# Kernel tuning notes

Measured on AMD Instinct MI355X. Metric: run time of the kernel, lower is better.

Reference implementation:

```python
import jax, jax.numpy as jnp
import numpy as np

KS = 5
STRIDE = 1


def extract_patches(x, ks, s):
    # TF tf.image.extract_patches ordering: (row, col, channel) flattened
    B, H, W, C = x.shape
    oh = (H - ks) // s + 1
    ow = (W - ks) // s + 1
    cols = [x[:, i:i + (oh - 1) * s + 1:s, j:j + (ow - 1) * s + 1:s, :]
            for i in range(ks) for j in range(ks)]
    p = jnp.stack(cols, axis=3)  # [B, oh, ow, ks*ks, C]
    return p.reshape(B, oh * ow, ks * ks * C)


def setup_inputs() -> dict:
    key = jax.random.key(0)
    k1, k2, k3 = jax.random.split(key, 3)
    B, H, W, C, K = 32, 14, 14, 32, 64
    mu_in = jax.random.normal(k1, (B, H, W, C), dtype=jnp.float32)
    Sigma_in = jax.random.uniform(k2, (B, H * W, H * W, C), dtype=jnp.float32)
    w_mu = 0.05 * jax.random.normal(k3, (KS, KS, C, K), dtype=jnp.float32)
    w_sigma = jnp.full((K,), -2.2, dtype=jnp.float32)
    return {"mu_in": mu_in, "Sigma_in": Sigma_in, "w_mu": w_mu, "w_sigma": w_sigma}


def reference(mu_in, Sigma_in, w_mu, w_sigma):
    B, H, W, C = mu_in.shape
    ks = w_mu.shape[0]
    K = w_mu.shape[-1]
    s = STRIDE

    # mean path: standard conv2d, NHWC / HWIO
    mu_out = jax.lax.conv_general_dilated(
        mu_in, w_mu, (s, s), 'VALID',
        dimension_numbers=('NHWC', 'HWIO', 'NHWC'))

    # diag of Sigma_in over the two N dims: [B,N,N,C] -> [B,C,N] -> [B,H,W,C]
    diag_sigma = jnp.diagonal(Sigma_in, axis1=1, axis2=2)           # [B,C,N]
    diag_sigma = jnp.transpose(diag_sigma, (0, 2, 1)).reshape(B, H, W, C)

    dsg = extract_patches(diag_sigma, ks, s)                        # [B,P,M]
    P = dsg.shape[1]

    mu_cov_sq = (w_mu * w_mu).reshape(-1, K)                        # [M,K]
    v1 = dsg @ mu_cov_sq                                            # [B,P,K]

    sp = jnp.log1p(jnp.exp(w_sigma))                                # softplus, [K]
    tr = jnp.sum(dsg, axis=2, keepdims=True)                        # [B,P,1]
    diag_vals = v1 + sp[None, None, :] * tr                         # [B,P,K] (trace1 + mu_wT_sigmags_mu_w diags)

    mu_p = extract_patches(mu_in, ks, s)                            # [B,P,M]
    G = jnp.einsum('bpm,bqm->bpq', mu_p, mu_p)                      # [B,P,P]

    Sigma_out = sp[None, None, None, :] * G[..., None]              # [B,P,P,K]
    ip = jnp.arange(P)
    Sigma_out = Sigma_out.at[:, ip, ip, :].add(diag_vals)

    Sigma_out = jnp.where(jnp.isnan(Sigma_out), 0.0, Sigma_out)
    Sigma_out = jnp.where(jnp.isinf(Sigma_out), 0.0, Sigma_out)

    # TF set_diag acts on the LAST two dims ([P,K] inner matrices) -- reproduce exactly
    m = min(P, K)
    ii = jnp.arange(m)
    Sigma_out = Sigma_out.at[:, :, ii, ii].set(jnp.abs(Sigma_out[:, :, ii, ii]))
    return mu_out, Sigma_out
```

## Files before the change

kernel.cpp:

```cpp
#include <hip/hip_runtime.h>
#include <cmath>

typedef __attribute__((ext_vector_type(8))) short short8;
typedef __attribute__((ext_vector_type(4))) float f32x4;

#define NB 32
#define PP 100
#define KK 64
#define MU_OUT_SZ (NB*PP*KK)
#define LDAP 56

__device__ inline unsigned short f2bf(float f) {
  unsigned u = __builtin_bit_cast(unsigned, f);
  u += 0x7fffu + ((u >> 16) & 1u);
  return (unsigned short)(u >> 16);
}

__global__ __launch_bounds__(256) void prepW(
    const float* __restrict__ w_mu, const float* __restrict__ w_sigma,
    unsigned short* __restrict__ wf) {
  const int wid = blockIdx.x * 256 + threadIdx.x;
  const int kind = wid >= 6400 ? 1 : 0;
  const int fid = kind ? wid - 6400 : wid;
  const int ij = fid >> 8;
  const int rest = fid & 255;
  const int n = rest >> 6, l = rest & 63;
  const int col = n * 16 + (l & 15);
  const int m0 = ij * 32 + (l >> 4) * 8;
  const float sp = log1pf(expf(w_sigma[col]));
  unsigned short v[8];
#pragma unroll
  for (int i = 0; i < 8; ++i) {
    float wv = w_mu[(m0 + i) * 64 + col];
    float x = kind ? (wv * wv + sp) : wv;
    v[i] = f2bf(x);
  }
  uint4 pk;
  pk.x = v[0] | ((unsigned)v[1] << 16);
  pk.y = v[2] | ((unsigned)v[3] << 16);
  pk.z = v[4] | ((unsigned)v[5] << 16);
  pk.w = v[6] | ((unsigned)v[7] << 16);
  *(uint4*)(wf + (size_t)((ij * 8 + kind * 4 + n) * 64 + l) * 8) = pk;
}

__global__ __launch_bounds__(256) void fused(
    const float* __restrict__ mu_in, const float* __restrict__ Sigma_in,
    const float* __restrict__ w_sigma, const unsigned short* __restrict__ wf,
    float* __restrict__ out) {
  __shared__ unsigned short mu_sh[196 * LDAP];
  __shared__ unsigned short sd_sh[196 * LDAP];
  __shared__ float g_sh[16][100];
  __shared__ float dv_sh[16][64];
  const int r = blockIdx.x;
  const int zh = blockIdx.y;
  const int b = blockIdx.z;
  const int t = threadIdx.x, l = t & 63, w = t >> 6;
  const int laneP = l & 15, g16 = (l >> 4) * 8;
  const bool hasDv = (zh == 0) ? (r <= 3) : (r >= 4);

  const float4* mu4 = (const float4*)(mu_in + (size_t)b * 6272);
  for (int f = t; f < 1568; f += 256) {
    const float4 v = mu4[f];
    const int row = f >> 3, c = (f & 7) * 4;
    ushort4 pv;
    pv.x = f2bf(v.x); pv.y = f2bf(v.y); pv.z = f2bf(v.z); pv.w = f2bf(v.w);
    *(ushort4*)(mu_sh + row * LDAP + c) = pv;
  }
  if (hasDv) {
    for (int f = t; f < 1568; f += 256) {
      const int n = f >> 3, c = (f & 7) * 4;
      const float4 v = *(const float4*)(Sigma_in +
          ((size_t)(b * 196 + n) * 196 + n) * 32 + c);
      ushort4 pv;
      pv.x = f2bf(v.x); pv.y = f2bf(v.y); pv.z = f2bf(v.z); pv.w = f2bf(v.w);
      *(ushort4*)(sd_sh + n * LDAP + c) = pv;
    }
  }
  __syncthreads();

  const int gTile = (zh == 0) ? w : (w < 3 ? 4 + w : -1);
  const bool doMu = (zh == 1);
  const int nT = w;

  int pA = r * 16 + laneP; if (pA > 99) pA = 99;
  const int baseA = ((pA / 10) * 14 + (pA % 10)) * LDAP + g16;
  int gcol = 0, baseB = 0;
  if (gTile >= 0) {
    gcol = gTile * 16 + laneP;
    const int pc = gcol > 99 ? 99 : gcol;
    baseB = ((pc / 10) * 14 + (pc % 10)) * LDAP + g16;
  }
  f32x4 accG = {}, accM = {}, accD = {};
#pragma unroll
  for (int ij = 0; ij < 25; ++ij) {
    const int off = ((ij / 5) * 14 + (ij % 5)) * LDAP;
    const short8 fA = *(const short8*)(mu_sh + baseA + off);
    if (gTile >= 0) {
      const short8 fB = *(const short8*)(mu_sh + baseB + off);
      accG = __builtin_amdgcn_mfma_f32_16x16x32_bf16(fA, fB, accG, 0, 0, 0);
    }
    if (doMu) {
      const short8 bw = *(const short8*)(wf + (size_t)((ij * 8 + nT) * 64 + l) * 8);
      accM = __builtin_amdgcn_mfma_f32_16x16x32_bf16(fA, bw, accM, 0, 0, 0);
    }
    if (hasDv) {
      const short8 fS = *(const short8*)(sd_sh + baseA + off);
      const short8 b2 = *(const short8*)(wf + (size_t)((ij * 8 + 4 + nT) * 64 + l) * 8);
      accD = __builtin_amdgcn_mfma_f32_16x16x32_bf16(fS, b2, accD, 0, 0, 0);
    }
  }
  const int prow0 = (l >> 4) * 4;
  if (gTile >= 0 && gcol < 100) {
#pragma unroll
    for (int j = 0; j < 4; ++j) g_sh[prow0 + j][gcol] = accG[j];
  }
  if (doMu) {
    float* mo = out + (size_t)b * 6400;
    const int k = nT * 16 + laneP;
#pragma unroll
    for (int j = 0; j < 4; ++j) {
      const int p = r * 16 + prow0 + j;
      if (p < 100) mo[p * 64 + k] = accM[j];
    }
  }
  if (hasDv) {
    const int k = nT * 16 + laneP;
#pragma unroll
    for (int j = 0; j < 4; ++j) dv_sh[prow0 + j][k] = accD[j];
  }
  __syncthreads();

  const int nrows = (r == 6) ? 4 : 16;
  const int koff = (t & 15) * 4;
  const float4 wsv = *(const float4*)(w_sigma + koff);
  float4 sp4;
  sp4.x = log1pf(expf(wsv.x));
  sp4.y = log1pf(expf(wsv.y));
  sp4.z = log1pf(expf(wsv.z));
  sp4.w = log1pf(expf(wsv.w));
  const int p0 = r * 16;
  float* sig = out + MU_OUT_SZ + ((size_t)(b * 100 + p0) * 100) * 64;

  if (zh == 0) {
    const int total = nrows << 10;
    for (int l4 = t; l4 < total; l4 += 256) {
      const int prow = l4 >> 10, rem = l4 & 1023;
      const int q = rem >> 4;
      const float g = g_sh[prow][q];
      float4 v;
      v.x = sp4.x * g; v.y = sp4.y * g; v.z = sp4.z * g; v.w = sp4.w * g;
      if (q == p0 + prow) {
        const float4 dvv = *(const float4*)&dv_sh[prow][koff];
        v.x += dvv.x; v.y += dvv.y; v.z += dvv.z; v.w += dvv.w;
      }
      if (q == koff)     v.x = fabsf(v.x);
      if (q == koff + 1) v.y = fabsf(v.y);
      if (q == koff + 2) v.z = fabsf(v.z);
      if (q == koff + 3) v.w = fabsf(v.w);
      *(float4*)(sig + ((size_t)prow * 100 + q) * 64 + koff) = v;
    }
  } else {
    const int total = nrows * 576;
    for (int l4 = t; l4 < total; l4 += 256) {
      const int prow = l4 / 576, rem = l4 - prow * 576;
      const int q = 64 + (rem >> 4);
      const float g = g_sh[prow][q];
      float4 v;
      v.x = sp4.x * g; v.y = sp4.y * g; v.z = sp4.z * g; v.w = sp4.w * g;
      if (q == p0 + prow) {
        const float4 dvv = *(const float4*)&dv_sh[prow][koff];
        v.x += dvv.x; v.y += dvv.y; v.z += dvv.z; v.w += dvv.w;
      }
      *(float4*)(sig + ((size_t)prow * 100 + q) * 64 + koff) = v;
    }
  }
}

extern "C" void kernel_launch(void* const* d_in, const int* in_sizes, int n_in,
                              void* d_out, int out_size, void* d_ws, size_t ws_size,
                              hipStream_t stream) {
  const float* mu_in    = (const float*)d_in[0];
  const float* Sigma_in = (const float*)d_in[1];
  const float* w_mu     = (const float*)d_in[2];
  const float* w_sigma  = (const float*)d_in[3];
  float* out = (float*)d_out;
  unsigned short* wf = (unsigned short*)d_ws;

  prepW<<<50, 256, 0, stream>>>(w_mu, w_sigma, wf);
  fused<<<dim3(7, 2, NB), 256, 0, stream>>>(mu_in, Sigma_in, w_sigma, wf, out);
}
```

Baseline: 34.63 us.

## Split fused kernel into GEMM stage and grid-stride streaming writer kernel

The single fused kernel is split into two. A gemm kernel computes G, dv and mu_out with per-wave specialised MFMA tiles and writes them to workspace. A separate writer kernel then streams the large Sigma_out tensor with a flat grid-stride loop and nontemporal stores. The aim is to decouple the bandwidth-bound output write from the compute-bound GEMM so the write can use the whole GPU with coalesced stores. The cost is an extra launch plus a global round trip for G and dv.

```diff
diff --git a/kernel.cpp b/kernel.cpp
--- a/kernel.cpp
+++ b/kernel.cpp
@@ -5,10 +5,12 @@
 typedef __attribute__((ext_vector_type(4))) float f32x4;
 
 #define NB 32
-#define PP 100
-#define KK 64
-#define MU_OUT_SZ (NB*PP*KK)
+#define MU_OUT_SZ (NB*100*64)
 #define LDAP 56
+
+#define WS_WF 0
+#define WS_G  204800
+#define WS_DV 1484800
 
 __device__ inline unsigned short f2bf(float f) {
   unsigned u = __builtin_bit_cast(unsigned, f);
@@ -43,20 +45,15 @@
   *(uint4*)(wf + (size_t)((ij * 8 + kind * 4 + n) * 64 + l) * 8) = pk;
 }
 
-__global__ __launch_bounds__(256) void fused(
+__global__ __launch_bounds__(256) void gemm(
     const float* __restrict__ mu_in, const float* __restrict__ Sigma_in,
-    const float* __restrict__ w_sigma, const unsigned short* __restrict__ wf,
-    float* __restrict__ out) {
+    const unsigned short* __restrict__ wf,
+    float* __restrict__ G, float* __restrict__ dv, float* __restrict__ out) {
   __shared__ unsigned short mu_sh[196 * LDAP];
   __shared__ unsigned short sd_sh[196 * LDAP];
-  __shared__ float g_sh[16][100];
-  __shared__ float dv_sh[16][64];
   const int r = blockIdx.x;
-  const int zh = blockIdx.y;
-  const int b = blockIdx.z;
+  const int b = blockIdx.y;
   const int t = threadIdx.x, l = t & 63, w = t >> 6;
-  const int laneP = l & 15, g16 = (l >> 4) * 8;
-  const bool hasDv = (zh == 0) ? (r <= 3) : (r >= 4);
 
   const float4* mu4 = (const float4*)(mu_in + (size_t)b * 6272);
   for (int f = t; f < 1568; f += 256) {
@@ -65,114 +62,127 @@
     ushort4 pv;
     pv.x = f2bf(v.x); pv.y = f2bf(v.y); pv.z = f2bf(v.z); pv.w = f2bf(v.w);
     *(ushort4*)(mu_sh + row * LDAP + c) = pv;
-  }
-  if (hasDv) {
-    for (int f = t; f < 1568; f += 256) {
-      const int n = f >> 3, c = (f & 7) * 4;
-      const float4 v = *(const float4*)(Sigma_in +
-          ((size_t)(b * 196 + n) * 196 + n) * 32 + c);
-      ushort4 pv;
-      pv.x = f2bf(v.x); pv.y = f2bf(v.y); pv.z = f2bf(v.z); pv.w = f2bf(v.w);
-      *(ushort4*)(sd_sh + n * LDAP + c) = pv;
-    }
+    const float4 s = *(const float4*)(Sigma_in +
+        ((size_t)(b * 196 + row) * 196 + row) * 32 + c);
+    ushort4 ps;
+    ps.x = f2bf(s.x); ps.y = f2bf(s.y); ps.z = f2bf(s.z); ps.w = f2bf(s.w);
+    *(ushort4*)(sd_sh + row * LDAP + c) = ps;
   }
   __syncthreads();
 
-  const int gTile = (zh == 0) ? w : (w < 3 ? 4 + w : -1);
-  const bool doMu = (zh == 1);
-  const int nT = w;
-
+  const int laneP = l & 15, g16 = (l >> 4) * 8;
   int pA = r * 16 + laneP; if (pA > 99) pA = 99;
   const int baseA = ((pA / 10) * 14 + (pA % 10)) * LDAP + g16;
-  int gcol = 0, baseB = 0;
-  if (gTile >= 0) {
-    gcol = gTile * 16 + laneP;
-    const int pc = gcol > 99 ? 99 : gcol;
-    baseB = ((pc / 10) * 14 + (pc % 10)) * LDAP + g16;
-  }
-  f32x4 accG = {}, accM = {}, accD = {};
-#pragma unroll
-  for (int ij = 0; ij < 25; ++ij) {
-    const int off = ((ij / 5) * 14 + (ij % 5)) * LDAP;
-    const short8 fA = *(const short8*)(mu_sh + baseA + off);
-    if (gTile >= 0) {
-      const short8 fB = *(const short8*)(mu_sh + baseB + off);
-      accG = __builtin_amdgcn_mfma_f32_16x16x32_bf16(fA, fB, accG, 0, 0, 0);
-    }
-    if (doMu) {
-      const short8 bw = *(const short8*)(wf + (size_t)((ij * 8 + nT) * 64 + l) * 8);
-      accM = __builtin_amdgcn_mfma_f32_16x16x32_bf16(fA, bw, accM, 0, 0, 0);
-    }
-    if (hasDv) {
+  const int prow0 = (l >> 4) * 4;
+
+  if (w <= 1) {
+    const int c0 = w * 4;
+    int baseB[4];
+#pragma unroll
+    for (int i = 0; i < 4; ++i) {
+      int col = (c0 + i) * 16 + laneP;
+      int pc = col > 99 ? 99 : col;
+      baseB[i] = ((pc / 10) * 14 + (pc % 10)) * LDAP + g16;
+    }
+    f32x4 acc[4] = {};
+#pragma unroll
+    for (int ij = 0; ij < 25; ++ij) {
+      const int off = ((ij / 5) * 14 + (ij % 5)) * LDAP;
+      const short8 fA = *(const short8*)(mu_sh + baseA + off);
+#pragma unroll
+      for (int i = 0; i < 4; ++i) {
+        const short8 fB = *(const short8*)(mu_sh + baseB[i] + off);
+        acc[i] = __builtin_amdgcn_mfma_f32_16x16x32_bf16(fA, fB, acc[i], 0, 0, 0);
+      }
+    }
+    float* Gb = G + (size_t)b * 10000;
+#pragma unroll
+    for (int i = 0; i < 4; ++i) {
+      const int col = (c0 + i) * 16 + laneP;
+      if (col < 100) {
+#pragma unroll
+        for (int j = 0; j < 4; ++j) {
+          const int row = r * 16 + prow0 + j;
+          if (row < 100) Gb[row * 100 + col] = acc[i][j];
+        }
+      }
+    }
+  } else if (w == 2) {
+    f32x4 acc[4] = {};
+#pragma unroll
+    for (int ij = 0; ij < 25; ++ij) {
+      const int off = ((ij / 5) * 14 + (ij % 5)) * LDAP;
+      const short8 fA = *(const short8*)(mu_sh + baseA + off);
+#pragma unroll
+      for (int n = 0; n < 4; ++n) {
+        const short8 bw = *(const short8*)(wf + (size_t)((ij * 8 + n) * 64 + l) * 8);
+        acc[n] = __builtin_amdgcn_mfma_f32_16x16x32_bf16(fA, bw, acc[n], 0, 0, 0);
+      }
+    }
+    float* mo = out + (size_t)b * 6400;
+#pragma unroll
+    for (int n = 0; n < 4; ++n) {
+      const int k = n * 16 + laneP;
+#pragma unroll
+      for (int j = 0; j < 4; ++j) {
+        const int p = r * 16 + prow0 + j;
+        if (p < 100) mo[p * 64 + k] = acc[n][j];
+      }
+    }
+  } else {
+    f32x4 acc[4] = {};
+#pragma unroll
+    for (int ij = 0; ij < 25; ++ij) {
+      const int off = ((ij / 5) * 14 + (ij % 5)) * LDAP;
       const short8 fS = *(const short8*)(sd_sh + baseA + off);
-      const short8 b2 = *(const short8*)(wf + (size_t)((ij * 8 + 4 + nT) * 64 + l) * 8);
-      accD = __builtin_amdgcn_mfma_f32_16x16x32_bf16(fS, b2, accD, 0, 0, 0);
-    }
-  }
-  const int prow0 = (l >> 4) * 4;
-  if (gTile >= 0 && gcol < 100) {
-#pragma unroll
-    for (int j = 0; j < 4; ++j) g_sh[prow0 + j][gcol] = accG[j];
-  }
-  if (doMu) {
-    float* mo = out + (size_t)b * 6400;
-    const int k = nT * 16 + laneP;
-#pragma unroll
-    for (int j = 0; j < 4; ++j) {
-      const int p = r * 16 + prow0 + j;
-      if (p < 100) mo[p * 64 + k] = accM[j];
-    }
-  }
-  if (hasDv) {
-    const int k = nT * 16 + laneP;
-#pragma unroll
-    for (int j = 0; j < 4; ++j) dv_sh[prow0 + j][k] = accD[j];
-  }
-  __syncthreads();
-
-  const int nrows = (r == 6) ? 4 : 16;
-  const int koff = (t & 15) * 4;
-  const float4 wsv = *(const float4*)(w_sigma + koff);
-  float4 sp4;
+#pragma unroll
+      for (int n = 0; n < 4; ++n) {
+        const short8 b2 = *(const short8*)(wf + (size_t)((ij * 8 + 4 + n) * 64 + l) * 8);
+        acc[n] = __builtin_amdgcn_mfma_f32_16x16x32_bf16(fS, b2, acc[n], 0, 0, 0);
+      }
+    }
+    float* dvb = dv + (size_t)b * 6400;
+#pragma unroll
+    for (int n = 0; n < 4; ++n) {
+      const int k = n * 16 + laneP;
+#pragma unroll
+      for (int j = 0; j < 4; ++j) {
+        const int p = r * 16 + prow0 + j;
+        if (p < 100) dvb[p * 64 + k] = acc[n][j];
+      }
+    }
+  }
+}
+
+__global__ __launch_bounds__(256) void writer(
+    const float* __restrict__ G, const float* __restrict__ dv,
+    const float* __restrict__ w_sigma, float* __restrict__ out) {
+  const unsigned tid = blockIdx.x * 256 + threadIdx.x;
+  const int k4 = (tid & 15) * 4;
+  const float4 wsv = *(const float4*)(w_sigma + k4);
+  f32x4 sp4;
   sp4.x = log1pf(expf(wsv.x));
   sp4.y = log1pf(expf(wsv.y));
   sp4.z = log1pf(expf(wsv.z));
   sp4.w = log1pf(expf(wsv.w));
-  const int p0 = r * 16;
-  float* sig = out + MU_OUT_SZ + ((size_t)(b * 100 + p0) * 100) * 64;
-
-  if (zh == 0) {
-    const int total = nrows << 10;
-    for (int l4 = t; l4 < total; l4 += 256) {
-      const int prow = l4 >> 10, rem = l4 & 1023;
-      const int q = rem >> 4;
-      const float g = g_sh[prow][q];
-      float4 v;
-      v.x = sp4.x * g; v.y = sp4.y * g; v.z = sp4.z * g; v.w = sp4.w * g;
-      if (q == p0 + prow) {
-        const float4 dvv = *(const float4*)&dv_sh[prow][koff];
-        v.x += dvv.x; v.y += dvv.y; v.z += dvv.z; v.w += dvv.w;
-      }
-      if (q == koff)     v.x = fabsf(v.x);
-      if (q == koff + 1) v.y = fabsf(v.y);
-      if (q == koff + 2) v.z = fabsf(v.z);
-      if (q == koff + 3) v.w = fabsf(v.w);
-      *(float4*)(sig + ((size_t)prow * 100 + q) * 64 + koff) = v;
-    }
-  } else {
-    const int total = nrows * 576;
-    for (int l4 = t; l4 < total; l4 += 256) {
-      const int prow = l4 / 576, rem = l4 - prow * 576;
-      const int q = 64 + (rem >> 4);
-      const float g = g_sh[prow][q];
-      float4 v;
-      v.x = sp4.x * g; v.y = sp4.y * g; v.z = sp4.z * g; v.w = sp4.w * g;
-      if (q == p0 + prow) {
-        const float4 dvv = *(const float4*)&dv_sh[prow][koff];
-        v.x += dvv.x; v.y += dvv.y; v.z += dvv.z; v.w += dvv.w;
-      }
-      *(float4*)(sig + ((size_t)prow * 100 + q) * 64 + koff) = v;
-    }
+  float* sig = out + MU_OUT_SZ;
+  for (unsigned l4 = tid; l4 < 5120000u; l4 += 524288u) {
+    const unsigned rr = l4 >> 4;
+    const unsigned q = rr % 100u;
+    const unsigned pq = rr / 100u;
+    const unsigned p = pq % 100u;
+    const float g = G[rr];
+    f32x4 v;
+    v.x = sp4.x * g; v.y = sp4.y * g; v.z = sp4.z * g; v.w = sp4.w * g;
+    if (q == p) {
+      const float4 dvv = *(const float4*)(dv + (size_t)pq * 64 + k4);
+      v.x += dvv.x; v.y += dvv.y; v.z += dvv.z; v.w += dvv.w;
+    }
+    v.x = (q == (unsigned)k4)     ? fabsf(v.x) : v.x;
+    v.y = (q == (unsigned)k4 + 1) ? fabsf(v.y) : v.y;
+    v.z = (q == (unsigned)k4 + 2) ? fabsf(v.z) : v.z;
+    v.w = (q == (unsigned)k4 + 3) ? fabsf(v.w) : v.w;
+    __builtin_nontemporal_store(v, (f32x4*)(sig + (size_t)l4 * 4));
   }
 }
 
@@ -184,8 +194,12 @@
   const float* w_mu     = (const float*)d_in[2];
   const float* w_sigma  = (const float*)d_in[3];
   float* out = (float*)d_out;
-  unsigned short* wf = (unsigned short*)d_ws;
+  unsigned char* ws = (unsigned char*)d_ws;
+  unsigned short* wf = (unsigned short*)(ws + WS_WF);
+  float* G  = (float*)(ws + WS_G);
+  float* dv = (float*)(ws + WS_DV);
 
   prepW<<<50, 256, 0, stream>>>(w_mu, w_sigma, wf);
-  fused<<<dim3(7, 2, NB), 256, 0, stream>>>(mu_in, Sigma_in, w_sigma, wf, out);
-}
+  gemm<<<dim3(7, NB), 256, 0, stream>>>(mu_in, Sigma_in, wf, G, dv, out);
+  writer<<<2048, 256, 0, stream>>>(G, dv, w_sigma, out);
+}
```

After: 37.00 us. 6.8% more time.

## Repartition fused kernel into two-row blocks across fifty tiles per batch

Applied to the files above, without the earlier changes.

The grid changes from 7x2 blocks per batch to 50 blocks per batch, and each block now handles two output rows p. Each block loads only the five image rows of the Sigma diagonal it needs, and every block computes the G, mu-conv and diag MFMAs, keeping only 2 of the 16 MFMA rows. The large Sigma_out write is spread over many more blocks and uses nontemporal stores. The cost is redundant per-block work: full mu staging and MFMAs that mostly go to waste in every block.

```diff
diff --git a/kernel.cpp b/kernel.cpp
--- a/kernel.cpp
+++ b/kernel.cpp
@@ -5,9 +5,7 @@
 typedef __attribute__((ext_vector_type(4))) float f32x4;
 
 #define NB 32
-#define PP 100
-#define KK 64
-#define MU_OUT_SZ (NB*PP*KK)
+#define MU_OUT_SZ (NB*100*64)
 #define LDAP 56
 
 __device__ inline unsigned short f2bf(float f) {
@@ -43,20 +41,19 @@
   *(uint4*)(wf + (size_t)((ij * 8 + kind * 4 + n) * 64 + l) * 8) = pk;
 }
 
-__global__ __launch_bounds__(256) void fused(
+__global__ __launch_bounds__(256) void fused2(
     const float* __restrict__ mu_in, const float* __restrict__ Sigma_in,
     const float* __restrict__ w_sigma, const unsigned short* __restrict__ wf,
     float* __restrict__ out) {
   __shared__ unsigned short mu_sh[196 * LDAP];
-  __shared__ unsigned short sd_sh[196 * LDAP];
-  __shared__ float g_sh[16][100];
-  __shared__ float dv_sh[16][64];
-  const int r = blockIdx.x;
-  const int zh = blockIdx.y;
-  const int b = blockIdx.z;
+  __shared__ unsigned short sd_sh[70 * LDAP];
+  __shared__ float g_sh[2][100];
+  __shared__ float dv_sh[2][64];
+  const int s = blockIdx.x;
+  const int b = blockIdx.y;
   const int t = threadIdx.x, l = t & 63, w = t >> 6;
-  const int laneP = l & 15, g16 = (l >> 4) * 8;
-  const bool hasDv = (zh == 0) ? (r <= 3) : (r >= 4);
+  const int p0 = 2 * s;
+  const int ph = p0 / 10;
 
   const float4* mu4 = (const float4*)(mu_in + (size_t)b * 6272);
   for (int f = t; f < 1568; f += 256) {
@@ -66,113 +63,86 @@
     pv.x = f2bf(v.x); pv.y = f2bf(v.y); pv.z = f2bf(v.z); pv.w = f2bf(v.w);
     *(ushort4*)(mu_sh + row * LDAP + c) = pv;
   }
-  if (hasDv) {
-    for (int f = t; f < 1568; f += 256) {
-      const int n = f >> 3, c = (f & 7) * 4;
-      const float4 v = *(const float4*)(Sigma_in +
-          ((size_t)(b * 196 + n) * 196 + n) * 32 + c);
-      ushort4 pv;
-      pv.x = f2bf(v.x); pv.y = f2bf(v.y); pv.z = f2bf(v.z); pv.w = f2bf(v.w);
-      *(ushort4*)(sd_sh + n * LDAP + c) = pv;
+  for (int f = t; f < 560; f += 256) {
+    const int hl = f / 112;
+    const int rem = f - hl * 112;
+    const int ww = rem >> 3, c = (rem & 7) * 4;
+    const int n = (ph + hl) * 14 + ww;
+    const float4 v = *(const float4*)(Sigma_in +
+        ((size_t)(b * 196 + n) * 196 + n) * 32 + c);
+    ushort4 pv;
+    pv.x = f2bf(v.x); pv.y = f2bf(v.y); pv.z = f2bf(v.z); pv.w = f2bf(v.w);
+    *(ushort4*)(sd_sh + (hl * 14 + ww) * LDAP + c) = pv;
+  }
+  __syncthreads();
+
+  const int laneP = l & 15, g16 = (l >> 4) * 8;
+  const int pA = (p0 + laneP > 99) ? 99 : p0 + laneP;
+  const int baseA = ((pA / 10) * 14 + (pA % 10)) * LDAP + g16;
+  const int pS = p0 + (laneP < 2 ? laneP : 1);
+  const int baseS = (pS % 10) * LDAP + g16;
+  const int tile0 = w;
+  const int tile1 = (w < 3) ? w + 4 : -1;
+  int q0 = tile0 * 16 + laneP; const int q0c = q0 > 99 ? 99 : q0;
+  const int baseB0 = ((q0c / 10) * 14 + (q0c % 10)) * LDAP + g16;
+  int q1 = 0, baseB1 = 0;
+  if (tile1 >= 0) {
+    q1 = tile1 * 16 + laneP; const int q1c = q1 > 99 ? 99 : q1;
+    baseB1 = ((q1c / 10) * 14 + (q1c % 10)) * LDAP + g16;
+  }
+  f32x4 aG0 = {}, aG1 = {}, aM = {}, aD = {};
+#pragma unroll
+  for (int ij = 0; ij < 25; ++ij) {
+    const int off = ((ij / 5) * 14 + (ij % 5)) * LDAP;
+    const short8 fA = *(const short8*)(mu_sh + baseA + off);
+    const short8 fB0 = *(const short8*)(mu_sh + baseB0 + off);
+    aG0 = __builtin_amdgcn_mfma_f32_16x16x32_bf16(fA, fB0, aG0, 0, 0, 0);
+    if (tile1 >= 0) {
+      const short8 fB1 = *(const short8*)(mu_sh + baseB1 + off);
+      aG1 = __builtin_amdgcn_mfma_f32_16x16x32_bf16(fA, fB1, aG1, 0, 0, 0);
+    }
+    const short8 bw = *(const short8*)(wf + (size_t)((ij * 8 + w) * 64 + l) * 8);
+    aM = __builtin_amdgcn_mfma_f32_16x16x32_bf16(fA, bw, aM, 0, 0, 0);
+    const short8 fS = *(const short8*)(sd_sh + baseS + off);
+    const short8 b2 = *(const short8*)(wf + (size_t)((ij * 8 + 4 + w) * 64 + l) * 8);
+    aD = __builtin_amdgcn_mfma_f32_16x16x32_bf16(fS, b2, aD, 0, 0, 0);
+  }
+  if (l < 16) {
+#pragma unroll
+    for (int j = 0; j < 2; ++j) {
+      if (q0 < 100) g_sh[j][q0] = aG0[j];
+      if (tile1 >= 0 && q1 < 100) g_sh[j][q1] = aG1[j];
+      const int k = w * 16 + laneP;
+      out[((size_t)b * 100 + p0 + j) * 64 + k] = aM[j];
+      dv_sh[j][k] = aD[j];
     }
   }
   __syncthreads();
 
-  const int gTile = (zh == 0) ? w : (w < 3 ? 4 + w : -1);
-  const bool doMu = (zh == 1);
-  const int nT = w;
-
-  int pA = r * 16 + laneP; if (pA > 99) pA = 99;
-  const int baseA = ((pA / 10) * 14 + (pA % 10)) * LDAP + g16;
-  int gcol = 0, baseB = 0;
-  if (gTile >= 0) {
-    gcol = gTile * 16 + laneP;
-    const int pc = gcol > 99 ? 99 : gcol;
-    baseB = ((pc / 10) * 14 + (pc % 10)) * LDAP + g16;
-  }
-  f32x4 accG = {}, accM = {}, accD = {};
-#pragma unroll
-  for (int ij = 0; ij < 25; ++ij) {
-    const int off = ((ij / 5) * 14 + (ij % 5)) * LDAP;
-    const short8 fA = *(const short8*)(mu_sh + baseA + off);
-    if (gTile >= 0) {
-      const short8 fB = *(const short8*)(mu_sh + baseB + off);
-      accG = __builtin_amdgcn_mfma_f32_16x16x32_bf16(fA, fB, accG, 0, 0, 0);
-    }
-    if (doMu) {
-      const short8 bw = *(const short8*)(wf + (size_t)((ij * 8 + nT) * 64 + l) * 8);
-      accM = __builtin_amdgcn_mfma_f32_16x16x32_bf16(fA, bw, accM, 0, 0, 0);
-    }
-    if (hasDv) {
-      const short8 fS = *(const short8*)(sd_sh + baseA + off);
-      const short8 b2 = *(const short8*)(wf + (size_t)((ij * 8 + 4 + nT) * 64 + l) * 8);
-      accD = __builtin_amdgcn_mfma_f32_16x16x32_bf16(fS, b2, accD, 0, 0, 0);
-    }
-  }
-  const int prow0 = (l >> 4) * 4;
-  if (gTile >= 0 && gcol < 100) {
-#pragma unroll
-    for (int j = 0; j < 4; ++j) g_sh[prow0 + j][gcol] = accG[j];
-  }
-  if (doMu) {
-    float* mo = out + (size_t)b * 6400;
-    const int k = nT * 16 + laneP;
-#pragma unroll
-    for (int j = 0; j < 4; ++j) {
-      const int p = r * 16 + prow0 + j;
-      if (p < 100) mo[p * 64 + k] = accM[j];
-    }
-  }
-  if (hasDv) {
-    const int k = nT * 16 + laneP;
-#pragma unroll
-    for (int j = 0; j < 4; ++j) dv_sh[prow0 + j][k] = accD[j];
-  }
-  __syncthreads();
-
-  const int nrows = (r == 6) ? 4 : 16;
-  const int koff = (t & 15) * 4;
-  const float4 wsv = *(const float4*)(w_sigma + koff);
-  float4 sp4;
+  const int k4 = (t & 15) * 4;
+  const float4 wsv = *(const float4*)(w_sigma + k4);
+  f32x4 sp4;
   sp4.x = log1pf(expf(wsv.x));
   sp4.y = log1pf(expf(wsv.y));
   sp4.z = log1pf(expf(wsv.z));
   sp4.w = log1pf(expf(wsv.w));
-  const int p0 = r * 16;
   float* sig = out + MU_OUT_SZ + ((size_t)(b * 100 + p0) * 100) * 64;
-
-  if (zh == 0) {
-    const int total = nrows << 10;
-    for (int l4 = t; l4 < total; l4 += 256) {
-      const int prow = l4 >> 10, rem = l4 & 1023;
-      const int q = rem >> 4;
-      const float g = g_sh[prow][q];
-      float4 v;
-      v.x = sp4.x * g; v.y = sp4.y * g; v.z = sp4.z * g; v.w = sp4.w * g;
-      if (q == p0 + prow) {
-        const float4 dvv = *(const float4*)&dv_sh[prow][koff];
-        v.x += dvv.x; v.y += dvv.y; v.z += dvv.z; v.w += dvv.w;
-      }
-      if (q == koff)     v.x = fabsf(v.x);
-      if (q == koff + 1) v.y = fabsf(v.y);
-      if (q == koff + 2) v.z = fabsf(v.z);
-      if (q == koff + 3) v.w = fabsf(v.w);
-      *(float4*)(sig + ((size_t)prow * 100 + q) * 64 + koff) = v;
+  for (int l4 = t; l4 < 3200; l4 += 256) {
+    const int row = (l4 >= 1600) ? 1 : 0;
+    const int rem = l4 - row * 1600;
+    const int q = rem >> 4;
+    const float g = g_sh[row][q];
+    f32x4 v;
+    v.x = sp4.x * g; v.y = sp4.y * g; v.z = sp4.z * g; v.w = sp4.w * g;
+    if (q == p0 + row) {
+      const float4 dvv = *(const float4*)&dv_sh[row][k4];
+      v.x += dvv.x; v.y += dvv.y; v.z += dvv.z; v.w += dvv.w;
     }
-  } else {
-    const int total = nrows * 576;
-    for (int l4 = t; l4 < total; l4 += 256) {
-      const int prow = l4 / 576, rem = l4 - prow * 576;
-      const int q = 64 + (rem >> 4);
-      const float g = g_sh[prow][q];
-      float4 v;
-      v.x = sp4.x * g; v.y = sp4.y * g; v.z = sp4.z * g; v.w = sp4.w * g;
-      if (q == p0 + prow) {
-        const float4 dvv = *(const float4*)&dv_sh[prow][koff];
-        v.x += dvv.x; v.y += dvv.y; v.z += dvv.z; v.w += dvv.w;
-      }
-      *(float4*)(sig + ((size_t)prow * 100 + q) * 64 + koff) = v;
-    }
+    v.x = (q == k4)     ? fabsf(v.x) : v.x;
+    v.y = (q == k4 + 1) ? fabsf(v.y) : v.y;
+    v.z = (q == k4 + 2) ? fabsf(v.z) : v.z;
+    v.w = (q == k4 + 3) ? fabsf(v.w) : v.w;
+    __builtin_nontemporal_store(v, (f32x4*)(sig + (size_t)l4 * 4));
   }
 }
 
@@ -187,5 +157,5 @@
   unsigned short* wf = (unsigned short*)d_ws;
 
   prepW<<<50, 256, 0, stream>>>(w_mu, w_sigma, wf);
-  fused<<<dim3(7, 2, NB), 256, 0, stream>>>(mu_in, Sigma_in, w_sigma, wf, out);
+  fused2<<<dim3(50, NB), 256, 0, stream>>>(mu_in, Sigma_in, w_sigma, wf, out);
 }
```

Result: slower. 42.96 us (+24.1%).
